# Optimization experiments

Hardware: AMD Instinct MI355X
Metric: run time of the kernel (lower is better)

The kernel has to match this reference:

```python
import jax, jax.numpy as jnp
import numpy as np

GN_GROUPS = 32
GN_EPS = 1e-5


def conv3x3(x, w, b=None):
    # x: [B,C,H,W], w: [O,I,3,3]
    y = jax.lax.conv_general_dilated(x, w, (1, 1), 'SAME',
                                     dimension_numbers=('NCHW', 'OIHW', 'NCHW'))
    if b is not None:
        y = y + b[None, :, None, None]
    return y


def group_norm(x, gamma, beta):
    B, C, H, W = x.shape
    xg = x.reshape(B, GN_GROUPS, C // GN_GROUPS, H, W)
    mu = xg.mean(axis=(2, 3, 4), keepdims=True)
    var = ((xg - mu) ** 2).mean(axis=(2, 3, 4), keepdims=True)
    xn = ((xg - mu) * jax.lax.rsqrt(var + GN_EPS)).reshape(B, C, H, W)
    return xn * gamma[None, :, None, None] + beta[None, :, None, None]


def tower(x, ws, gammas, betas):
    # ws: [n_conv, C, C, 3, 3]; conv(bias=False) -> GroupNorm -> ReLU, n_conv times
    for i in range(ws.shape[0]):
        x = jax.nn.relu(group_norm(conv3x3(x, ws[i]), gammas[i], betas[i]))
    return x


def setup_inputs() -> dict:
    key = jax.random.key(0)
    ks = jax.random.split(key, 20)
    C, n_conv, n_fg = 256, 4, 20  # n_class - 1 = 20
    prior = 0.01
    B = 2
    sizes = [(100, 100), (50, 50), (25, 25), (13, 13), (7, 7)]
    inp = {}
    for i, (h, w) in enumerate(sizes):
        inp[f'feat{i}'] = jax.random.normal(ks[i], (B, C, h, w), dtype=jnp.float32)
    std = 0.01  # init_conv_std
    inp['cls_tw_w'] = std * jax.random.normal(ks[5], (n_conv, C, C, 3, 3), dtype=jnp.float32)
    inp['cls_tw_g'] = jnp.ones((n_conv, C), dtype=jnp.float32)
    inp['cls_tw_b'] = jnp.zeros((n_conv, C), dtype=jnp.float32)
    inp['box_tw_w'] = std * jax.random.normal(ks[6], (n_conv, C, C, 3, 3), dtype=jnp.float32)
    inp['box_tw_g'] = jnp.ones((n_conv, C), dtype=jnp.float32)
    inp['box_tw_b'] = jnp.zeros((n_conv, C), dtype=jnp.float32)
    inp['cls_pred_w'] = std * jax.random.normal(ks[7], (n_fg, C, 3, 3), dtype=jnp.float32)
    prior_bias = -np.log((1.0 - prior) / prior)
    inp['cls_pred_b'] = jnp.full((n_fg,), prior_bias, dtype=jnp.float32)
    inp['box_pred_w'] = std * jax.random.normal(ks[8], (4, C, 3, 3), dtype=jnp.float32)
    inp['box_pred_b'] = jnp.zeros((4,), dtype=jnp.float32)
    inp['ctr_pred_w'] = std * jax.random.normal(ks[9], (1, C, 3, 3), dtype=jnp.float32)
    inp['ctr_pred_b'] = jnp.zeros((1,), dtype=jnp.float32)
    inp['scales'] = jnp.ones((5,), dtype=jnp.float32)
    return inp


def reference(feat0, feat1, feat2, feat3, feat4,
              cls_tw_w, cls_tw_g, cls_tw_b,
              box_tw_w, box_tw_g, box_tw_b,
              cls_pred_w, cls_pred_b,
              box_pred_w, box_pred_b,
              ctr_pred_w, ctr_pred_b,
              scales):
    feats = [feat0, feat1, feat2, feat3, feat4]
    logits, bboxes, centers = [], [], []
    for i, feat in enumerate(feats):
        c = tower(feat, cls_tw_w, cls_tw_g, cls_tw_b)
        logits.append(conv3x3(c, cls_pred_w, cls_pred_b))
        centers.append(conv3x3(c, ctr_pred_w, ctr_pred_b))
        b = tower(feat, box_tw_w, box_tw_g, box_tw_b)
        bboxes.append(jnp.exp(conv3x3(b, box_pred_w, box_pred_b) * scales[i]))
    return tuple(logits + bboxes + centers)
```

## Files before the change

### kernel.cpp

```cpp
#include <hip/hip_runtime.h>
#include <hip/hip_bf16.h>
#include <cstdint>

typedef unsigned short u16;
typedef __attribute__((ext_vector_type(8))) short short8;
typedef __attribute__((ext_vector_type(4))) float floatx4;
typedef __attribute__((ext_vector_type(4))) int intx4;

#define PA_TOTAL 13696
#define CCH 256
#define KTOT 2304

struct Tables {
  int H[5], W[5], P[5], base[5], tile0[5];
  int lb[5], bb[5], cb[5];
};
struct FeatPtrs { const float* f[5]; };
struct ConvArgs {
  const u16* X[2];
  const u16* Wt[2];
  const u16* zbuf;
  u16* outB[2];
  float* stats;
  float* dout;
  const float* biasCls; const float* biasCtr; const float* biasBox; const float* scales;
};

__device__ __forceinline__ u16 f2bf(float f) {
  union { float f; unsigned u; } v; v.f = f;
  unsigned r = v.u + 0x7fffu + ((v.u >> 16) & 1u);
  return (u16)(r >> 16);
}
__device__ __forceinline__ float bf2f(u16 h) {
  union { unsigned u; float f; } v; v.u = ((unsigned)h) << 16;
  return v.f;
}

__global__ void reorder_rows(const float* __restrict__ src, u16* __restrict__ out) {
  __shared__ float row[KTOT];
  const int r = blockIdx.x;
  const float* s = src + (size_t)r * KTOT;
  u16* o = out + (size_t)r * KTOT;
#pragma unroll
  for (int j = 0; j < 9; ++j) row[threadIdx.x + j * 256] = s[threadIdx.x + j * 256];
  __syncthreads();
#pragma unroll
  for (int j = 0; j < 9; ++j) {
    int k = threadIdx.x + j * 256;
    o[k] = f2bf(row[(k & 255) * 9 + (k >> 8)]);
  }
}

__global__ void reorder_pred_cls(const float* __restrict__ cls_w, const float* __restrict__ ctr_w,
                                 u16* __restrict__ out) {
  __shared__ float row[KTOT];
  const int r = blockIdx.x;
  const float* s = (r < 20) ? (cls_w + (size_t)r * KTOT) : ctr_w;
  u16* o = out + (size_t)r * KTOT;
#pragma unroll
  for (int j = 0; j < 9; ++j) row[threadIdx.x + j * 256] = s[threadIdx.x + j * 256];
  __syncthreads();
#pragma unroll
  for (int j = 0; j < 9; ++j) {
    int k = threadIdx.x + j * 256;
    o[k] = f2bf(row[(k & 255) * 9 + (k >> 8)]);
  }
}

__global__ void convert_inputs(FeatPtrs fp, u16* __restrict__ out, Tables tb) {
  __shared__ float tile[32][33];
  const int pt = blockIdx.x, c32 = blockIdx.y, b = blockIdx.z;
  const int p0 = pt * 32;
  int lvl = 0;
#pragma unroll
  for (int i = 1; i < 5; ++i) if (p0 >= tb.base[i]) lvl = i;
  const int P = tb.P[lvl];
  const int pl0 = p0 - tb.base[lvl];
  const int r = threadIdx.x >> 5, col = threadIdx.x & 31;
  const float* src = fp.f[lvl] + ((size_t)b * CCH + c32 * 32) * P;
#pragma unroll
  for (int i = 0; i < 4; ++i) {
    int crow = r + i * 8;
    int pl = pl0 + col;
    tile[crow][col] = (pl < P) ? src[(size_t)crow * P + pl] : 0.f;
  }
  __syncthreads();
#pragma unroll
  for (int i = 0; i < 4; ++i) {
    int px = r + i * 8;
    out[((size_t)b * PA_TOTAL + p0 + px) * CCH + c32 * 32 + col] = f2bf(tile[col][px]);
  }
}

template <int MODE>
__global__ __launch_bounds__(256) void conv_mfma(ConvArgs a, Tables tb) {
  constexpr int NI = (MODE == 0) ? 4 : 1;
  const int L = blockIdx.x + (MODE == 0 ? 107 : 108) * (blockIdx.y + 2 * blockIdx.z);
  const int xcd = L & 7, slot = L >> 3;
  int tower, mt, b, t;
  if (MODE == 0) {
    tower = xcd >> 2; mt = (xcd >> 1) & 1; b = xcd & 1; t = slot;
  } else {
    tower = xcd >> 2; mt = 0; b = (xcd >> 1) & 1; t = slot * 2 + (xcd & 1);
    if (t >= 107) return;
  }
  int lvl = 0;
#pragma unroll
  for (int i = 1; i < 5; ++i) if (t >= tb.tile0[i]) lvl = i;
  const int H = tb.H[lvl], W = tb.W[lvl], P = tb.P[lvl], base = tb.base[lvl];
  const int n0 = (t - tb.tile0[lvl]) * 128;

  const int tid = threadIdx.x;
  const int lane = tid & 63, wv = tid >> 6;
  const int wm = wv >> 1, wn = wv & 1;

  __shared__ u16 ldsX[128 * 64];
  __shared__ u16 ldsW[(MODE == 0 ? 128 : 32) * 64];

  const u16* X = a.X[tower];
  const u16* Wt = a.Wt[tower];

  const int qsw = (((lane & 7) ^ (lane >> 3))) * 8;
  int prow[4];
  unsigned mask9[4];
  int xdst[4];
#pragma unroll
  for (int t4 = 0; t4 < 4; ++t4) {
    int row = (t4 * 4 + wv) * 8 + (lane >> 3);
    prow[t4] = n0 + row;
    int rr = prow[t4] / W, cc = prow[t4] - rr * W;
    unsigned m = 0;
#pragma unroll
    for (int tap = 0; tap < 9; ++tap) {
      const int dh = tap / 3 - 1, dw = tap % 3 - 1;
      bool v = ((unsigned)(rr + dh) < (unsigned)H) & ((unsigned)(cc + dw) < (unsigned)W);
      m |= ((unsigned)v) << tap;
    }
    mask9[t4] = m;
    xdst[t4] = (t4 * 4 + wv) * 1024 + lane * 16;
  }
  const u16* wsrc[NI];
  int wdst[NI];
#pragma unroll
  for (int e = 0; e < NI; ++e) {
    int wrow = (MODE == 0) ? ((e * 4 + wv) * 8 + (lane >> 3)) : (wv * 8 + (lane >> 3));
    wsrc[e] = Wt + (size_t)(mt * 128 + wrow) * KTOT + qsw;
    wdst[e] = (MODE == 0) ? xdst[e] : (wv * 1024 + lane * 16);
  }
  const u16* Xbp = X + ((size_t)b * PA_TOTAL + base) * CCH;

  const int arow = lane & 15, rsw = lane & 7, kq0 = lane >> 4;
  int aoff[2][NI], boff[2][4];
#pragma unroll
  for (int h = 0; h < 2; ++h) {
    int csw = (((h * 4 + kq0) ^ rsw)) * 8;
#pragma unroll
    for (int i = 0; i < NI; ++i) {
      int rowb = (MODE == 0) ? (wm * 64 + i * 16) : (wm * 16);
      aoff[h][i] = (rowb + arow) * 64 + csw;
    }
#pragma unroll
    for (int i = 0; i < 4; ++i) boff[h][i] = (wn * 64 + i * 16 + arow) * 64 + csw;
  }

  floatx4 acc[NI][4];
#pragma unroll
  for (int i = 0; i < NI; ++i)
#pragma unroll
    for (int j = 0; j < 4; ++j) acc[i][j] = (floatx4)0.f;

  const intx4 zreg = {0, 0, 0, 0};
  intx4 xr[4], wr[NI];
  {
    const int dpos0 = -W - 1;
#pragma unroll
    for (int t4 = 0; t4 < 4; ++t4)
      xr[t4] = (mask9[t4] & 1)
          ? *(const intx4*)(Xbp + (size_t)(prow[t4] + dpos0) * CCH + qsw) : zreg;
#pragma unroll
    for (int e = 0; e < NI; ++e) wr[e] = *(const intx4*)(wsrc[e]);
  }

#pragma unroll 1
  for (int icb = 0; icb < 4; ++icb) {
#pragma unroll
    for (int tap = 0; tap < 9; ++tap) {
      __syncthreads();
#pragma unroll
      for (int t4 = 0; t4 < 4; ++t4) *(intx4*)((char*)ldsX + xdst[t4]) = xr[t4];
#pragma unroll
      for (int e = 0; e < NI; ++e) *(intx4*)((char*)ldsW + wdst[e]) = wr[e];
      if (!(icb == 3 && tap == 8)) {
        const int ntap = (tap == 8) ? 0 : tap + 1;
        const int nicb = (tap == 8) ? icb + 1 : icb;
        const int ndh = ntap / 3;
        const int ndpos = (ndh - 1) * W + (ntap - 3 * ndh - 1);
        const int nko = ntap * 256 + nicb * 64;
#pragma unroll
        for (int t4 = 0; t4 < 4; ++t4)
          xr[t4] = ((mask9[t4] >> ntap) & 1)
              ? *(const intx4*)(Xbp + (size_t)(prow[t4] + ndpos) * CCH + qsw + nicb * 64) : zreg;
#pragma unroll
        for (int e = 0; e < NI; ++e) wr[e] = *(const intx4*)(wsrc[e] + nko);
      }
      __syncthreads();
#pragma unroll
      for (int h = 0; h < 2; ++h) {
        short8 af[NI], bv[4];
#pragma unroll
        for (int i = 0; i < NI; ++i) af[i] = *(const short8*)(ldsW + aoff[h][i]);
#pragma unroll
        for (int j = 0; j < 4; ++j) bv[j] = *(const short8*)(ldsX + boff[h][j]);
#pragma unroll
        for (int i = 0; i < NI; ++i)
#pragma unroll
          for (int j = 0; j < 4; ++j)
            acc[i][j] = __builtin_amdgcn_mfma_f32_16x16x32_bf16(af[i], bv[j], acc[i][j], 0, 0, 0);
      }
    }
  }

  const int quad = lane >> 4, col = lane & 15;
  if (MODE == 0) {
    u16* convB = a.outB[tower];
    float s[4] = {0.f, 0.f, 0.f, 0.f}, ss[4] = {0.f, 0.f, 0.f, 0.f};
#pragma unroll
    for (int j = 0; j < 4; ++j) {
      int pl = n0 + wn * 64 + j * 16 + col;
      bool valid = pl < P;
      u16* dst = convB + ((size_t)b * PA_TOTAL + base + pl) * CCH + mt * 128 + wm * 64 + quad * 4;
#pragma unroll
      for (int i = 0; i < 4; ++i) {
        ushort4 hv;
#pragma unroll
        for (int r = 0; r < 4; ++r) {
          u16 hh = f2bf(acc[i][j][r]);
          ((u16*)&hv)[r] = hh;
          float vr = bf2f(hh);
          if (valid) { s[i] += vr; ss[i] += vr * vr; }
        }
        if (valid) *(ushort4*)(dst + i * 16) = hv;
      }
    }
#pragma unroll
    for (int i = 0; i < 4; ++i) {
#pragma unroll
      for (int off = 16; off >= 1; off >>= 1) {
        s[i] += __shfl_down(s[i], off, 64);
        ss[i] += __shfl_down(ss[i], off, 64);
      }
    }
    if ((lane & 31) == 0) {
      int half = lane >> 5;
#pragma unroll
      for (int i = 0; i < 4; ++i) {
        float* st = a.stats + tower * 640 +
                    ((size_t)((b * 5 + lvl) * 32 + mt * 16 + wm * 8 + i * 2 + half)) * 2;
        atomicAdd(st, s[i]);
        atomicAdd(st + 1, ss[i]);
      }
    }
  } else {
    float* dout = a.dout;
    if (tower == 0) {
#pragma unroll
      for (int j = 0; j < 4; ++j) {
        int pl = n0 + wn * 64 + j * 16 + col;
        if (pl >= P) continue;
        int ocb = wm * 16 + quad * 4;
#pragma unroll
        for (int r = 0; r < 4; ++r) {
          int oc = ocb + r;
          float v = acc[0][j][r];
          if (oc < 20)       dout[tb.lb[lvl] + ((size_t)b * 20 + oc) * P + pl] = v + a.biasCls[oc];
          else if (oc == 20) dout[tb.cb[lvl] + (size_t)b * P + pl] = v + a.biasCtr[0];
        }
      }
    } else {
      float sc = a.scales[lvl];
#pragma unroll
      for (int j = 0; j < 4; ++j) {
        int pl = n0 + wn * 64 + j * 16 + col;
        if (pl >= P) continue;
        int ocb = wm * 16 + quad * 4;
#pragma unroll
        for (int r = 0; r < 4; ++r) {
          int oc = ocb + r;
          if (oc < 4)
            dout[tb.bb[lvl] + ((size_t)b * 4 + oc) * P + pl] = expf((acc[0][j][r] + a.biasBox[oc]) * sc);
        }
      }
    }
  }
}

__global__ void gn_norm(const u16* __restrict__ c0, const u16* __restrict__ c1,
                        const float* __restrict__ stats,
                        const float* __restrict__ g0, const float* __restrict__ b0,
                        const float* __restrict__ g1, const float* __restrict__ b1,
                        u16* __restrict__ a0, u16* __restrict__ a1, Tables tb) {
  const int tower = blockIdx.y;
  const u16* convB = tower ? c1 : c0;
  const float* gamma = tower ? g1 : g0;
  const float* beta = tower ? b1 : b0;
  u16* act = tower ? a1 : a0;
  int idx = blockIdx.x * 256 + threadIdx.x;
  int c8 = idx & 31;
  int rest = idx >> 5;
  int p = rest % PA_TOTAL;
  int b = rest / PA_TOTAL;
  int lvl = 0;
#pragma unroll
  for (int i = 1; i < 5; ++i) if (p >= tb.base[i]) lvl = i;
  if (p - tb.base[lvl] >= tb.P[lvl]) return;
  const float* st = stats + tower * 640 + ((size_t)((b * 5 + lvl) * 32 + c8)) * 2;
  float cnt = 8.f * (float)tb.P[lvl];
  float mean = st[0] / cnt;
  float var = st[1] / cnt - mean * mean;
  float inv = rsqrtf(var + 1e-5f);
  const short8 x = *(const short8*)(convB + ((size_t)b * PA_TOTAL + p) * CCH + c8 * 8);
  short8 o;
#pragma unroll
  for (int j = 0; j < 8; ++j) {
    float v = bf2f((u16)x[j]);
    float y = (v - mean) * inv * gamma[c8 * 8 + j] + beta[c8 * 8 + j];
    y = fmaxf(y, 0.f);
    o[j] = (short)f2bf(y);
  }
  *(short8*)(act + ((size_t)b * PA_TOTAL + p) * CCH + c8 * 8) = o;
}

extern "C" void kernel_launch(void* const* d_in, const int* in_sizes, int n_in,
                              void* d_out, int out_size, void* d_ws, size_t ws_size,
                              hipStream_t stream) {
  const float* feat[5];
  for (int i = 0; i < 5; ++i) feat[i] = (const float*)d_in[i];
  const float* cls_tw_w  = (const float*)d_in[5];
  const float* cls_tw_g  = (const float*)d_in[6];
  const float* cls_tw_b  = (const float*)d_in[7];
  const float* box_tw_w  = (const float*)d_in[8];
  const float* box_tw_g  = (const float*)d_in[9];
  const float* box_tw_b  = (const float*)d_in[10];
  const float* cls_pred_w = (const float*)d_in[11];
  const float* cls_pred_b = (const float*)d_in[12];
  const float* box_pred_w = (const float*)d_in[13];
  const float* box_pred_b = (const float*)d_in[14];
  const float* ctr_pred_w = (const float*)d_in[15];
  const float* ctr_pred_b = (const float*)d_in[16];
  const float* scales     = (const float*)d_in[17];
  float* out = (float*)d_out;

  char* ws = (char*)d_ws;
  u16*   zbuf   = (u16*)(ws);
  float* stats  = (float*)(ws + 512);
  u16*   WrCls  = (u16*)(ws + 8192);
  u16*   WrBox  = (u16*)(ws + 8192 + 4718592);
  u16*   WrPCls = (u16*)(ws + 8192 + 2 * 4718592);
  u16*   WrPBox = (u16*)(ws + 8192 + 2 * 4718592 + 589824);
  u16*   bufIn   = (u16*)(ws + 10625024);
  u16*   bufAct0 = (u16*)(ws + 10625024 + 1 * (size_t)14024704);
  u16*   bufAct1 = (u16*)(ws + 10625024 + 2 * (size_t)14024704);
  u16*   bufCv0  = (u16*)(ws + 10625024 + 3 * (size_t)14024704);
  u16*   bufCv1  = (u16*)(ws + 10625024 + 4 * (size_t)14024704);

  Tables tb = { {100,50,25,13,7}, {100,50,25,13,7}, {10000,2500,625,169,49},
                {0,10112,12672,13312,13568}, {0,79,99,104,106},
                {0,400000,500000,525000,531760},
                {533720,613720,633720,638720,640072},
                {640464,660464,665464,666714,667052} };

  hipMemsetAsync(zbuf, 0, 512, stream);
  hipMemsetAsync(WrPCls, 0, 589824, stream);
  hipMemsetAsync(WrPBox, 0, 589824, stream);

  reorder_rows<<<1024, 256, 0, stream>>>(cls_tw_w, WrCls);
  reorder_rows<<<1024, 256, 0, stream>>>(box_tw_w, WrBox);
  reorder_pred_cls<<<21, 256, 0, stream>>>(cls_pred_w, ctr_pred_w, WrPCls);
  reorder_rows<<<4, 256, 0, stream>>>(box_pred_w, WrPBox);

  FeatPtrs fp = {{feat[0], feat[1], feat[2], feat[3], feat[4]}};
  convert_inputs<<<dim3(PA_TOTAL / 32, 8, 2), 256, 0, stream>>>(fp, bufIn, tb);

  ConvArgs a;
  a.zbuf = zbuf; a.stats = stats; a.dout = out;
  a.biasCls = cls_pred_b; a.biasCtr = ctr_pred_b; a.biasBox = box_pred_b; a.scales = scales;
  a.outB[0] = bufCv0; a.outB[1] = bufCv1;

  for (int s = 0; s < 4; ++s) {
    a.X[0] = (s == 0) ? bufIn : bufAct0;
    a.X[1] = (s == 0) ? bufIn : bufAct1;
    a.Wt[0] = WrCls + (size_t)s * 256 * KTOT;
    a.Wt[1] = WrBox + (size_t)s * 256 * KTOT;
    hipMemsetAsync(stats, 0, 5120, stream);
    conv_mfma<0><<<dim3(107, 2, 4), 256, 0, stream>>>(a, tb);
    gn_norm<<<dim3(3424, 2), 256, 0, stream>>>(bufCv0, bufCv1, stats,
                                               cls_tw_g + s * 256, cls_tw_b + s * 256,
                                               box_tw_g + s * 256, box_tw_b + s * 256,
                                               bufAct0, bufAct1, tb);
  }
  a.X[0] = bufAct0; a.X[1] = bufAct1;
  a.Wt[0] = WrPCls; a.Wt[1] = WrPBox;
  conv_mfma<1><<<dim3(108, 2, 2), 256, 0, stream>>>(a, tb);
}
```

Measured before the change: 639.6 us.

## Double-buffer conv tiles in LDS with direct global-to-LDS loads

Replaces the register-staged global load and LDS store with global_load_lds direct-to-LDS transfers into double-buffered LDS tiles. Out-of-bounds halo taps read from a zero buffer instead of being selected in registers. The next tap's tiles are prefetched while the current one is consumed, gated by explicit vmcnt waits and raw barriers, and MFMA sections run at raised wave priority. This is meant to cut register pressure and overlap global latency with compute, at the cost of doubled LDS use and reliance on hand-placed waitcnt and barrier ordering.

```diff
diff --git a/kernel.cpp b/kernel.cpp
--- a/kernel.cpp
+++ b/kernel.cpp
@@ -36,6 +36,12 @@
   return v.f;
 }
 
+__device__ __forceinline__ void gload16(const void* g, void* l) {
+  __builtin_amdgcn_global_load_lds(
+      (const __attribute__((address_space(1))) void*)g,
+      (__attribute__((address_space(3))) void*)l, 16, 0, 0);
+}
+
 __global__ void reorder_rows(const float* __restrict__ src, u16* __restrict__ out) {
   __shared__ float row[KTOT];
   const int r = blockIdx.x;
@@ -95,6 +101,8 @@
 template <int MODE>
 __global__ __launch_bounds__(256) void conv_mfma(ConvArgs a, Tables tb) {
   constexpr int NI = (MODE == 0) ? 4 : 1;
+  constexpr int WROWS = (MODE == 0) ? 128 : 32;
+  constexpr int NLOADS = NI + 4;
   const int L = blockIdx.x + (MODE == 0 ? 107 : 108) * (blockIdx.y + 2 * blockIdx.z);
   const int xcd = L & 7, slot = L >> 3;
   int tower, mt, b, t;
@@ -114,8 +122,8 @@
   const int lane = tid & 63, wv = tid >> 6;
   const int wm = wv >> 1, wn = wv & 1;
 
-  __shared__ u16 ldsX[128 * 64];
-  __shared__ u16 ldsW[(MODE == 0 ? 128 : 32) * 64];
+  __shared__ u16 ldsX[2][128 * 64];
+  __shared__ u16 ldsW[2][WROWS * 64];
 
   const u16* X = a.X[tower];
   const u16* Wt = a.Wt[tower];
@@ -123,7 +131,7 @@
   const int qsw = (((lane & 7) ^ (lane >> 3))) * 8;
   int prow[4];
   unsigned mask9[4];
-  int xdst[4];
+  int xoff[4];
 #pragma unroll
   for (int t4 = 0; t4 < 4; ++t4) {
     int row = (t4 * 4 + wv) * 8 + (lane >> 3);
@@ -137,17 +145,18 @@
       m |= ((unsigned)v) << tap;
     }
     mask9[t4] = m;
-    xdst[t4] = (t4 * 4 + wv) * 1024 + lane * 16;
+    xoff[t4] = (t4 * 4 + wv) * 1024;
   }
   const u16* wsrc[NI];
-  int wdst[NI];
+  int woff[NI];
 #pragma unroll
   for (int e = 0; e < NI; ++e) {
     int wrow = (MODE == 0) ? ((e * 4 + wv) * 8 + (lane >> 3)) : (wv * 8 + (lane >> 3));
     wsrc[e] = Wt + (size_t)(mt * 128 + wrow) * KTOT + qsw;
-    wdst[e] = (MODE == 0) ? xdst[e] : (wv * 1024 + lane * 16);
+    woff[e] = (MODE == 0) ? ((e * 4 + wv) * 1024) : (wv * 1024);
   }
   const u16* Xbp = X + ((size_t)b * PA_TOTAL + base) * CCH;
+  const u16* zsrc = a.zbuf;
 
   const int arow = lane & 15, rsw = lane & 7, kq0 = lane >> 4;
   int aoff[2][NI], boff[2][4];
@@ -169,54 +178,63 @@
 #pragma unroll
     for (int j = 0; j < 4; ++j) acc[i][j] = (floatx4)0.f;
 
-  const intx4 zreg = {0, 0, 0, 0};
-  intx4 xr[4], wr[NI];
   {
     const int dpos0 = -W - 1;
 #pragma unroll
-    for (int t4 = 0; t4 < 4; ++t4)
-      xr[t4] = (mask9[t4] & 1)
-          ? *(const intx4*)(Xbp + (size_t)(prow[t4] + dpos0) * CCH + qsw) : zreg;
-#pragma unroll
-    for (int e = 0; e < NI; ++e) wr[e] = *(const intx4*)(wsrc[e]);
-  }
-
+    for (int t4 = 0; t4 < 4; ++t4) {
+      const u16* s = (mask9[t4] & 1)
+          ? (Xbp + (size_t)(prow[t4] + dpos0) * CCH + qsw) : zsrc;
+      gload16(s, (char*)&ldsX[0][0] + xoff[t4]);
+    }
+#pragma unroll
+    for (int e = 0; e < NI; ++e) gload16(wsrc[e], (char*)&ldsW[0][0] + woff[e]);
+  }
+
+  int pbuf = 0;
 #pragma unroll 1
   for (int icb = 0; icb < 4; ++icb) {
 #pragma unroll
     for (int tap = 0; tap < 9; ++tap) {
-      __syncthreads();
-#pragma unroll
-      for (int t4 = 0; t4 < 4; ++t4) *(intx4*)((char*)ldsX + xdst[t4]) = xr[t4];
-#pragma unroll
-      for (int e = 0; e < NI; ++e) *(intx4*)((char*)ldsW + wdst[e]) = wr[e];
       if (!(icb == 3 && tap == 8)) {
         const int ntap = (tap == 8) ? 0 : tap + 1;
         const int nicb = (tap == 8) ? icb + 1 : icb;
         const int ndh = ntap / 3;
         const int ndpos = (ndh - 1) * W + (ntap - 3 * ndh - 1);
         const int nko = ntap * 256 + nicb * 64;
-#pragma unroll
-        for (int t4 = 0; t4 < 4; ++t4)
-          xr[t4] = ((mask9[t4] >> ntap) & 1)
-              ? *(const intx4*)(Xbp + (size_t)(prow[t4] + ndpos) * CCH + qsw + nicb * 64) : zreg;
-#pragma unroll
-        for (int e = 0; e < NI; ++e) wr[e] = *(const intx4*)(wsrc[e] + nko);
-      }
-      __syncthreads();
+        u16* xn = &ldsX[0][0] + (pbuf ^ 1) * (128 * 64);
+        u16* wn = &ldsW[0][0] + (pbuf ^ 1) * (WROWS * 64);
+#pragma unroll
+        for (int t4 = 0; t4 < 4; ++t4) {
+          const u16* s = ((mask9[t4] >> ntap) & 1)
+              ? (Xbp + (size_t)(prow[t4] + ndpos) * CCH + qsw + nicb * 64) : zsrc;
+          gload16(s, (char*)xn + xoff[t4]);
+        }
+#pragma unroll
+        for (int e = 0; e < NI; ++e) gload16(wsrc[e] + nko, (char*)wn + woff[e]);
+        asm volatile("s_waitcnt vmcnt(%0)" :: "n"(NLOADS) : "memory");
+      } else {
+        asm volatile("s_waitcnt vmcnt(0)" ::: "memory");
+      }
+      asm volatile("s_barrier" ::: "memory");
+      const u16* xc = &ldsX[0][0] + pbuf * (128 * 64);
+      const u16* wc = &ldsW[0][0] + pbuf * (WROWS * 64);
+      __builtin_amdgcn_s_setprio(1);
 #pragma unroll
       for (int h = 0; h < 2; ++h) {
         short8 af[NI], bv[4];
 #pragma unroll
-        for (int i = 0; i < NI; ++i) af[i] = *(const short8*)(ldsW + aoff[h][i]);
-#pragma unroll
-        for (int j = 0; j < 4; ++j) bv[j] = *(const short8*)(ldsX + boff[h][j]);
+        for (int i = 0; i < NI; ++i) af[i] = *(const short8*)(wc + aoff[h][i]);
+#pragma unroll
+        for (int j = 0; j < 4; ++j) bv[j] = *(const short8*)(xc + boff[h][j]);
 #pragma unroll
         for (int i = 0; i < NI; ++i)
 #pragma unroll
           for (int j = 0; j < 4; ++j)
             acc[i][j] = __builtin_amdgcn_mfma_f32_16x16x32_bf16(af[i], bv[j], acc[i][j], 0, 0, 0);
       }
+      __builtin_amdgcn_s_setprio(0);
+      asm volatile("s_barrier" ::: "memory");
+      pbuf ^= 1;
     }
   }
 
```

Measured after the change: 922.2 us. 1.44x slower.
